# Kernel tuning notes

Hardware: AMD Instinct MI355X
Metric: run time of the kernel (lower is better)

Reference implementation:

```python
import jax, jax.numpy as jnp
import numpy as np

B, T, S, K, H, V = 8, 100, 400, 8, 512, 32000

def setup_inputs() -> dict:
    key = jax.random.key(0)
    ks = jax.random.split(key, 8)
    return {
        "dec_out": jax.random.normal(ks[0], (B, T, H), jnp.float32),
        "W": jax.random.normal(ks[1], (H, V), jnp.float32) * (1.0 / np.sqrt(H)),
        "b": jnp.zeros((V,), jnp.float32),
        "weights": jax.random.uniform(ks[2], (B, T, S), jnp.float32),
        "p_trans": jax.random.uniform(ks[3], (B, T, 1), jnp.float32),
        "trans_probs": jax.random.uniform(ks[4], (B, S, K), jnp.float32),
        "probs": jax.random.uniform(ks[5], (B, S, K), jnp.float32),
        "idxes": jax.random.randint(ks[6], (B, S, K), 0, V, jnp.int64),
    }

def reference(dec_out, W, b, weights, p_trans, trans_probs, probs, idxes):
    # Generator: linear + softmax over vocab -> (B, T, V)
    scores = jax.nn.softmax(jnp.einsum('bth,hv->btv', dec_out, W) + b, axis=-1)
    # Mask translation probs where source prob <= 0.05
    tp = trans_probs * (probs > 0.05).astype(trans_probs.dtype)  # (B, S, K)
    # scatter_add along vocab dim: tmp[b, s, idxes[b, s, k]] += tp[b, s, k]
    bi = jnp.arange(B)[:, None, None]
    si = jnp.arange(S)[None, :, None]
    tmp = jnp.zeros((B, S, V), dec_out.dtype).at[bi, si, idxes].add(tp)
    # blend copy distribution through attention weights
    trans_scores = jnp.einsum('bts,bsv->btv', weights, tmp)
    return jnp.log(p_trans * trans_scores + (1.0 - p_trans) * scores)
```

## Files before the change

kernel.cpp:

```cpp
#include <hip/hip_runtime.h>

#define Bdim 8
#define Tdim 100
#define Sdim 400
#define Kk   8
#define Hdim 512
#define Vdim 32000
#define Mdim 800
#define VHALF 16000

typedef __attribute__((ext_vector_type(8))) short short8;
typedef __attribute__((ext_vector_type(4))) float float4_t;

static __device__ __forceinline__ unsigned short f2bf(float f) {
    unsigned int x = __float_as_uint(f);
    return (unsigned short)((x + 0x7fffu + ((x >> 16) & 1u)) >> 16);
}
static __device__ __forceinline__ float bf2f(unsigned short h) {
    return __uint_as_float(((unsigned int)h) << 16);
}

static __device__ __forceinline__ void gload_lds16(const void* g, void* s) {
    __builtin_amdgcn_global_load_lds((const __attribute__((address_space(1))) void*)g,
                                     (__attribute__((address_space(3))) void*)s, 16, 0, 0);
}

__global__ void zero_kernel(float* __restrict__ p, int n) {
    int i = blockIdx.x * blockDim.x + threadIdx.x;
    if (i < n) p[i] = 0.f;
}

__global__ void convert_a_kernel(const float* __restrict__ A, unsigned short* __restrict__ Abf, int n) {
    int i = blockIdx.x * blockDim.x + threadIdx.x;
    if (i < n) Abf[i] = f2bf(A[i]);
}

__global__ void transpose_kernel(const float* __restrict__ W, unsigned short* __restrict__ WT) {
    __shared__ float tile[32][33];
    int k0 = blockIdx.y * 32;
    int v0 = blockIdx.x * 32;
    int tx = threadIdx.x & 31;
    int ty = threadIdx.x >> 5;
#pragma unroll
    for (int i = 0; i < 32; i += 8)
        tile[ty + i][tx] = W[(k0 + ty + i) * Vdim + v0 + tx];
    __syncthreads();
#pragma unroll
    for (int i = 0; i < 32; i += 8) {
        int v = v0 + ty + i;
        WT[v * Hdim + k0 + tx] = f2bf(tile[tx][ty + i]);
    }
}

__global__ __launch_bounds__(256) void gemm_kernel(const unsigned short* __restrict__ Abf,
                                                   const unsigned short* __restrict__ WT,
                                                   const float* __restrict__ bias,
                                                   unsigned short* __restrict__ logitsbf,
                                                   float* __restrict__ rowsum) {
    __shared__ __align__(16) unsigned short As[128 * 64];
    __shared__ __align__(16) unsigned short Bs[128 * 64];

    const int tid  = threadIdx.x;
    const int lane = tid & 63;
    const int wave = tid >> 6;
    const int l15  = lane & 15;
    const int kq   = lane >> 4;
    const int m_blk = blockIdx.x * 128;
    const int n_blk = blockIdx.y * 128;
    const int wm = wave & 1, wn = wave >> 1;
    const int m0 = wm * 64, n0 = wn * 64;

    const unsigned short* agp[4];
    const unsigned short* bgp[4];
    unsigned short* alp[4];
    unsigned short* blp[4];
#pragma unroll
    for (int q = 0; q < 4; ++q) {
        int chunk = (q * 4 + wave) * 64 + lane;
        int row = chunk >> 3, c = chunk & 7;
        int gc  = c ^ (row & 7);
        int arow = m_blk + row;
        if (arow >= Mdim) arow = Mdim - 1;
        agp[q] = Abf + (size_t)arow * Hdim + gc * 8;
        bgp[q] = WT + (size_t)(n_blk + row) * Hdim + gc * 8;
        alp[q] = As + (q * 4 + wave) * 512;
        blp[q] = Bs + (q * 4 + wave) * 512;
    }

    int a_off[2][4], b_off[2][4];
#pragma unroll
    for (int ks = 0; ks < 2; ++ks)
#pragma unroll
        for (int i = 0; i < 4; ++i) {
            int ra = m0 + i * 16 + l15;
            a_off[ks][i] = ra * 64 + (((ks * 4 + kq) ^ (ra & 7)) * 8);
            int rb = n0 + i * 16 + l15;
            b_off[ks][i] = rb * 64 + (((ks * 4 + kq) ^ (rb & 7)) * 8);
        }

    float4_t acc[4][4] = {};

    for (int kt = 0; kt < 8; ++kt) {
        if (kt) __syncthreads();
        const int ko = kt * 64;
#pragma unroll
        for (int q = 0; q < 4; ++q) {
            gload_lds16(agp[q] + ko, alp[q]);
            gload_lds16(bgp[q] + ko, blp[q]);
        }
        __syncthreads();
#pragma unroll
        for (int ks = 0; ks < 2; ++ks) {
            short8 af[4], bfr[4];
#pragma unroll
            for (int i = 0; i < 4; ++i) af[i]  = *(const short8*)(As + a_off[ks][i]);
#pragma unroll
            for (int j = 0; j < 4; ++j) bfr[j] = *(const short8*)(Bs + b_off[ks][j]);
#pragma unroll
            for (int i = 0; i < 4; ++i)
#pragma unroll
                for (int j = 0; j < 4; ++j)
                    acc[i][j] = __builtin_amdgcn_mfma_f32_16x16x32_bf16(af[i], bfr[j], acc[i][j], 0, 0, 0);
        }
    }

    float bj[4];
#pragma unroll
    for (int j = 0; j < 4; ++j) bj[j] = bias[n_blk + n0 + j * 16 + l15];

#pragma unroll
    for (int i = 0; i < 4; ++i) {
        float se[4] = {0.f, 0.f, 0.f, 0.f};
        int grow0 = m_blk + m0 + i * 16 + kq * 4;
#pragma unroll
        for (int j = 0; j < 4; ++j) {
            int col = n_blk + n0 + j * 16 + l15;
#pragma unroll
            for (int r = 0; r < 4; ++r) {
                float v = acc[i][j][r] + bj[j];
                se[r] += __expf(v);
                if (grow0 + r < Mdim)
                    logitsbf[(size_t)(grow0 + r) * Vdim + col] = f2bf(v);
            }
        }
#pragma unroll
        for (int r = 0; r < 4; ++r) {
#pragma unroll
            for (int off = 8; off; off >>= 1)
                se[r] += __shfl_xor(se[r], off, 64);
        }
        if (l15 == 0) {
#pragma unroll
            for (int r = 0; r < 4; ++r)
                if (grow0 + r < Mdim) atomicAdd(&rowsum[grow0 + r], se[r]);
        }
    }
}

__global__ __launch_bounds__(512) void combine_kernel(const unsigned short* __restrict__ logitsbf,
                                                      const float* __restrict__ weights,
                                                      const float* __restrict__ p_trans,
                                                      const float* __restrict__ trans_probs,
                                                      const float* __restrict__ probs,
                                                      const int* __restrict__ idxes,
                                                      const float* __restrict__ rowsum,
                                                      float* __restrict__ out) {
    __shared__ __align__(16) float ts[VHALF];

    int bt = blockIdx.x;
    int b  = bt / Tdim;
    int tid = threadIdx.x;

    float pt = p_trans[bt];
    float c1 = (1.f - pt) / rowsum[bt];

    const short8* lrow8 = (const short8*)(logitsbf + (size_t)bt * Vdim);
    float4* out4 = (float4*)(out + (size_t)bt * Vdim);
    float4* ts4  = (float4*)ts;

    for (int h = 0; h < 2; ++h) {
        float4 z = make_float4(0.f, 0.f, 0.f, 0.f);
        for (int i = tid; i < VHALF / 4; i += 512) ts4[i] = z;
        __syncthreads();

        for (int i = tid; i < Sdim * Kk; i += 512) {
            float pv  = probs[b * (Sdim * Kk) + i];
            float tpv = trans_probs[b * (Sdim * Kk) + i];
            int   idx = idxes[b * (Sdim * Kk) + i];
            int   rel = idx - h * VHALF;
            if (pv > 0.05f && (unsigned)rel < (unsigned)VHALF) {
                float w = weights[bt * Sdim + (i >> 3)];
                atomicAdd(&ts[rel], w * tpv);
            }
        }
        __syncthreads();

        for (int i = tid; i < VHALF / 8; i += 512) {
            short8 x8 = lrow8[h * (VHALF / 8) + i];
            float4 t0 = ts4[i * 2];
            float4 t1 = ts4[i * 2 + 1];
            float4 o0, o1;
            o0.x = __logf(pt * t0.x + c1 * __expf(bf2f((unsigned short)x8[0])));
            o0.y = __logf(pt * t0.y + c1 * __expf(bf2f((unsigned short)x8[1])));
            o0.z = __logf(pt * t0.z + c1 * __expf(bf2f((unsigned short)x8[2])));
            o0.w = __logf(pt * t0.w + c1 * __expf(bf2f((unsigned short)x8[3])));
            o1.x = __logf(pt * t1.x + c1 * __expf(bf2f((unsigned short)x8[4])));
            o1.y = __logf(pt * t1.y + c1 * __expf(bf2f((unsigned short)x8[5])));
            o1.z = __logf(pt * t1.z + c1 * __expf(bf2f((unsigned short)x8[6])));
            o1.w = __logf(pt * t1.w + c1 * __expf(bf2f((unsigned short)x8[7])));
            out4[(h * (VHALF / 8) + i) * 2]     = o0;
            out4[(h * (VHALF / 8) + i) * 2 + 1] = o1;
        }
        __syncthreads();
    }
}

extern "C" void kernel_launch(void* const* d_in, const int* in_sizes, int n_in,
                              void* d_out, int out_size, void* d_ws, size_t ws_size,
                              hipStream_t stream) {
    const float* dec_out     = (const float*)d_in[0];
    const float* W           = (const float*)d_in[1];
    const float* bias        = (const float*)d_in[2];
    const float* weights     = (const float*)d_in[3];
    const float* p_trans     = (const float*)d_in[4];
    const float* trans_probs = (const float*)d_in[5];
    const float* probs       = (const float*)d_in[6];
    const int*   idxes       = (const int*)d_in[7];
    float* out = (float*)d_out;

    char* wsb = (char*)d_ws;
    unsigned short* Abf      = (unsigned short*)wsb;
    unsigned short* WT       = (unsigned short*)(wsb + (1ull << 20));
    unsigned short* logitsbf = (unsigned short*)(wsb + (35ull << 20));
    float*          rowsum   = (float*)(wsb + (90ull << 20));

    zero_kernel<<<dim3(4), dim3(256), 0, stream>>>(rowsum, Mdim);
    convert_a_kernel<<<dim3((Mdim * Hdim + 255) / 256), dim3(256), 0, stream>>>(dec_out, Abf, Mdim * Hdim);
    transpose_kernel<<<dim3(Vdim / 32, Hdim / 32), dim3(256), 0, stream>>>(W, WT);
    gemm_kernel<<<dim3(7, Vdim / 128), dim3(256), 0, stream>>>(Abf, WT, bias, logitsbf, rowsum);
    combine_kernel<<<dim3(Mdim), dim3(512), 0, stream>>>(logitsbf, weights, p_trans, trans_probs,
                                                         probs, idxes, rowsum, out);
}
```

Baseline: 294.2 us.

## Keep full W tile resident in LDS and stream pre-packed A fragments

The GEMM now launches one block per 128-column vocab tile and loads the whole 128x512 bf16 W slice into LDS once (128 KB). It then loops over all 7 M tiles, reading A directly from global memory in a pre-packed MFMA fragment layout produced by a rewritten convert kernel. This removes the repeated W reloads across M blocks and the per-k-step barriers. The cost is only 250 blocks with very large LDS use, so occupancy is one block per CU. Separately, the combine kernel keeps the full 32000-float vocab row in LDS and does a single pass instead of two halves, which also needs a large LDS allocation.

New measurement: 478.0 us. +62.5%, slower.

```diff
diff --git a/kernel.cpp b/kernel.cpp
--- a/kernel.cpp
+++ b/kernel.cpp
@@ -7,7 +7,6 @@
 #define Hdim 512
 #define Vdim 32000
 #define Mdim 800
-#define VHALF 16000
 
 typedef __attribute__((ext_vector_type(8))) short short8;
 typedef __attribute__((ext_vector_type(4))) float float4_t;
@@ -30,9 +29,18 @@
     if (i < n) p[i] = 0.f;
 }
 
-__global__ void convert_a_kernel(const float* __restrict__ A, unsigned short* __restrict__ Abf, int n) {
-    int i = blockIdx.x * blockDim.x + threadIdx.x;
-    if (i < n) Abf[i] = f2bf(A[i]);
+__global__ void convert_a_kernel(const float* __restrict__ A, unsigned short* __restrict__ Ap) {
+    int tid = blockIdx.x * blockDim.x + threadIdx.x;
+    if (tid >= 50 * 1024) return;
+    int mt = tid >> 10;
+    int r  = tid & 1023;
+    int kc = r >> 4;
+    int l15 = r & 15;
+    const float* src = A + (size_t)(mt * 16 + l15) * Hdim + kc * 8;
+    short8 v;
+#pragma unroll
+    for (int j = 0; j < 8; ++j) v[j] = (short)f2bf(src[j]);
+    *(short8*)(Ap + (size_t)tid * 8) = v;
 }
 
 __global__ void transpose_kernel(const float* __restrict__ W, unsigned short* __restrict__ WT) {
@@ -43,116 +51,105 @@
     int ty = threadIdx.x >> 5;
 #pragma unroll
     for (int i = 0; i < 32; i += 8)
-        tile[ty + i][tx] = W[(k0 + ty + i) * Vdim + v0 + tx];
+        tile[ty + i][tx] = W[(size_t)(k0 + ty + i) * Vdim + v0 + tx];
     __syncthreads();
 #pragma unroll
     for (int i = 0; i < 32; i += 8) {
         int v = v0 + ty + i;
-        WT[v * Hdim + k0 + tx] = f2bf(tile[tx][ty + i]);
-    }
-}
-
-__global__ __launch_bounds__(256) void gemm_kernel(const unsigned short* __restrict__ Abf,
+        WT[(size_t)v * Hdim + k0 + tx] = f2bf(tile[tx][ty + i]);
+    }
+}
+
+__global__ __launch_bounds__(256) void gemm_kernel(const unsigned short* __restrict__ Ap,
                                                    const unsigned short* __restrict__ WT,
                                                    const float* __restrict__ bias,
                                                    unsigned short* __restrict__ logitsbf,
                                                    float* __restrict__ rowsum) {
-    __shared__ __align__(16) unsigned short As[128 * 64];
-    __shared__ __align__(16) unsigned short Bs[128 * 64];
+    __shared__ __align__(16) unsigned short Bs[128 * 512];
 
     const int tid  = threadIdx.x;
     const int lane = tid & 63;
     const int wave = tid >> 6;
     const int l15  = lane & 15;
     const int kq   = lane >> 4;
-    const int m_blk = blockIdx.x * 128;
-    const int n_blk = blockIdx.y * 128;
+    const int n_blk = blockIdx.x * 128;
     const int wm = wave & 1, wn = wave >> 1;
-    const int m0 = wm * 64, n0 = wn * 64;
-
-    const unsigned short* agp[4];
-    const unsigned short* bgp[4];
-    unsigned short* alp[4];
-    unsigned short* blp[4];
-#pragma unroll
-    for (int q = 0; q < 4; ++q) {
-        int chunk = (q * 4 + wave) * 64 + lane;
-        int row = chunk >> 3, c = chunk & 7;
-        int gc  = c ^ (row & 7);
-        int arow = m_blk + row;
-        if (arow >= Mdim) arow = Mdim - 1;
-        agp[q] = Abf + (size_t)arow * Hdim + gc * 8;
-        bgp[q] = WT + (size_t)(n_blk + row) * Hdim + gc * 8;
-        alp[q] = As + (q * 4 + wave) * 512;
-        blp[q] = Bs + (q * 4 + wave) * 512;
-    }
-
-    int a_off[2][4], b_off[2][4];
-#pragma unroll
-    for (int ks = 0; ks < 2; ++ks)
+    const int n0 = wn * 64;
+
+#pragma unroll 4
+    for (int it = 0; it < 32; ++it) {
+        int s = it * 256 + wave * 64 + lane;
+        int row = s >> 6, cs = s & 63;
+        int gc = (cs & 56) | ((cs & 7) ^ (row & 7));
+        gload_lds16(WT + (size_t)(n_blk + row) * Hdim + gc * 8,
+                    Bs + (size_t)(it * 256 + wave * 64) * 8);
+    }
+    __syncthreads();
+
+    int e0[4], e1[4];
+#pragma unroll
+    for (int j = 0; j < 4; ++j) {
+        int n = n0 + j * 16 + l15;
+        e0[j] = n * 512 + ((kq ^ (n & 7)) * 8);
+        e1[j] = n * 512 + (((4 + kq) ^ (n & 7)) * 8);
+    }
+
+    float bj[4];
+#pragma unroll
+    for (int j = 0; j < 4; ++j) bj[j] = bias[n_blk + n0 + j * 16 + l15];
+
+    for (int m_tile = 0; m_tile < 7; ++m_tile) {
+        const unsigned short* ap[4];
 #pragma unroll
         for (int i = 0; i < 4; ++i) {
-            int ra = m0 + i * 16 + l15;
-            a_off[ks][i] = ra * 64 + (((ks * 4 + kq) ^ (ra & 7)) * 8);
-            int rb = n0 + i * 16 + l15;
-            b_off[ks][i] = rb * 64 + (((ks * 4 + kq) ^ (rb & 7)) * 8);
-        }
-
-    float4_t acc[4][4] = {};
-
-    for (int kt = 0; kt < 8; ++kt) {
-        if (kt) __syncthreads();
-        const int ko = kt * 64;
-#pragma unroll
-        for (int q = 0; q < 4; ++q) {
-            gload_lds16(agp[q] + ko, alp[q]);
-            gload_lds16(bgp[q] + ko, blp[q]);
-        }
-        __syncthreads();
-#pragma unroll
-        for (int ks = 0; ks < 2; ++ks) {
+            int mt = m_tile * 8 + wm * 4 + i;
+            if (mt > 49) mt = 49;
+            ap[i] = Ap + (size_t)mt * 8192 + lane * 8;
+        }
+
+        float4_t acc[4][4] = {};
+#pragma unroll
+        for (int ks = 0; ks < 16; ++ks) {
             short8 af[4], bfr[4];
 #pragma unroll
-            for (int i = 0; i < 4; ++i) af[i]  = *(const short8*)(As + a_off[ks][i]);
-#pragma unroll
-            for (int j = 0; j < 4; ++j) bfr[j] = *(const short8*)(Bs + b_off[ks][j]);
+            for (int i = 0; i < 4; ++i) af[i] = *(const short8*)(ap[i] + ks * 512);
+            const int co = (ks >> 1) * 64;
+#pragma unroll
+            for (int j = 0; j < 4; ++j)
+                bfr[j] = *(const short8*)(Bs + ((ks & 1) ? e1[j] : e0[j]) + co);
 #pragma unroll
             for (int i = 0; i < 4; ++i)
 #pragma unroll
                 for (int j = 0; j < 4; ++j)
                     acc[i][j] = __builtin_amdgcn_mfma_f32_16x16x32_bf16(af[i], bfr[j], acc[i][j], 0, 0, 0);
         }
-    }
-
-    float bj[4];
-#pragma unroll
-    for (int j = 0; j < 4; ++j) bj[j] = bias[n_blk + n0 + j * 16 + l15];
-
-#pragma unroll
-    for (int i = 0; i < 4; ++i) {
-        float se[4] = {0.f, 0.f, 0.f, 0.f};
-        int grow0 = m_blk + m0 + i * 16 + kq * 4;
-#pragma unroll
-        for (int j = 0; j < 4; ++j) {
-            int col = n_blk + n0 + j * 16 + l15;
+
+#pragma unroll
+        for (int i = 0; i < 4; ++i) {
+            float se[4] = {0.f, 0.f, 0.f, 0.f};
+            int grow0 = m_tile * 128 + wm * 64 + i * 16 + kq * 4;
+#pragma unroll
+            for (int j = 0; j < 4; ++j) {
+                int col = n_blk + n0 + j * 16 + l15;
+#pragma unroll
+                for (int r = 0; r < 4; ++r) {
+                    float v = acc[i][j][r] + bj[j];
+                    se[r] += __expf(v);
+                    if (grow0 + r < Mdim)
+                        logitsbf[(size_t)(grow0 + r) * Vdim + col] = f2bf(v);
+                }
+            }
 #pragma unroll
             for (int r = 0; r < 4; ++r) {
-                float v = acc[i][j][r] + bj[j];
-                se[r] += __expf(v);
-                if (grow0 + r < Mdim)
-                    logitsbf[(size_t)(grow0 + r) * Vdim + col] = f2bf(v);
+#pragma unroll
+                for (int off = 8; off; off >>= 1)
+                    se[r] += __shfl_xor(se[r], off, 64);
             }
-        }
-#pragma unroll
-        for (int r = 0; r < 4; ++r) {
-#pragma unroll
-            for (int off = 8; off; off >>= 1)
-                se[r] += __shfl_xor(se[r], off, 64);
-        }
-        if (l15 == 0) {
-#pragma unroll
-            for (int r = 0; r < 4; ++r)
-                if (grow0 + r < Mdim) atomicAdd(&rowsum[grow0 + r], se[r]);
+            if (l15 == 0) {
+#pragma unroll
+                for (int r = 0; r < 4; ++r)
+                    if (grow0 + r < Mdim) atomicAdd(&rowsum[grow0 + r], se[r]);
+            }
         }
     }
 }
@@ -165,7 +162,7 @@
                                                       const int* __restrict__ idxes,
                                                       const float* __restrict__ rowsum,
                                                       float* __restrict__ out) {
-    __shared__ __align__(16) float ts[VHALF];
+    __shared__ __align__(16) float ts[Vdim];
 
     int bt = blockIdx.x;
     int b  = bt / Tdim;
@@ -178,40 +175,36 @@
     float4* out4 = (float4*)(out + (size_t)bt * Vdim);
     float4* ts4  = (float4*)ts;
 
-    for (int h = 0; h < 2; ++h) {
-        float4 z = make_float4(0.f, 0.f, 0.f, 0.f);
-        for (int i = tid; i < VHALF / 4; i += 512) ts4[i] = z;
-        __syncthreads();
-
-        for (int i = tid; i < Sdim * Kk; i += 512) {
-            float pv  = probs[b * (Sdim * Kk) + i];
-            float tpv = trans_probs[b * (Sdim * Kk) + i];
-            int   idx = idxes[b * (Sdim * Kk) + i];
-            int   rel = idx - h * VHALF;
-            if (pv > 0.05f && (unsigned)rel < (unsigned)VHALF) {
-                float w = weights[bt * Sdim + (i >> 3)];
-                atomicAdd(&ts[rel], w * tpv);
-            }
-        }
-        __syncthreads();
-
-        for (int i = tid; i < VHALF / 8; i += 512) {
-            short8 x8 = lrow8[h * (VHALF / 8) + i];
-            float4 t0 = ts4[i * 2];
-            float4 t1 = ts4[i * 2 + 1];
-            float4 o0, o1;
-            o0.x = __logf(pt * t0.x + c1 * __expf(bf2f((unsigned short)x8[0])));
-            o0.y = __logf(pt * t0.y + c1 * __expf(bf2f((unsigned short)x8[1])));
-            o0.z = __logf(pt * t0.z + c1 * __expf(bf2f((unsigned short)x8[2])));
-            o0.w = __logf(pt * t0.w + c1 * __expf(bf2f((unsigned short)x8[3])));
-            o1.x = __logf(pt * t1.x + c1 * __expf(bf2f((unsigned short)x8[4])));
-            o1.y = __logf(pt * t1.y + c1 * __expf(bf2f((unsigned short)x8[5])));
-            o1.z = __logf(pt * t1.z + c1 * __expf(bf2f((unsigned short)x8[6])));
-            o1.w = __logf(pt * t1.w + c1 * __expf(bf2f((unsigned short)x8[7])));
-            out4[(h * (VHALF / 8) + i) * 2]     = o0;
-            out4[(h * (VHALF / 8) + i) * 2 + 1] = o1;
-        }
-        __syncthreads();
+    float4 z = make_float4(0.f, 0.f, 0.f, 0.f);
+    for (int i = tid; i < Vdim / 4; i += 512) ts4[i] = z;
+    __syncthreads();
+
+    for (int i = tid; i < Sdim * Kk; i += 512) {
+        float pv  = probs[b * (Sdim * Kk) + i];
+        float tpv = trans_probs[b * (Sdim * Kk) + i];
+        int   idx = idxes[b * (Sdim * Kk) + i];
+        if (pv > 0.05f) {
+            float w = weights[bt * Sdim + (i >> 3)];
+            atomicAdd(&ts[idx], w * tpv);
+        }
+    }
+    __syncthreads();
+
+    for (int i = tid; i < Vdim / 8; i += 512) {
+        short8 x8 = lrow8[i];
+        float4 t0 = ts4[i * 2];
+        float4 t1 = ts4[i * 2 + 1];
+        float4 o0, o1;
+        o0.x = __logf(pt * t0.x + c1 * __expf(bf2f((unsigned short)x8[0])));
+        o0.y = __logf(pt * t0.y + c1 * __expf(bf2f((unsigned short)x8[1])));
+        o0.z = __logf(pt * t0.z + c1 * __expf(bf2f((unsigned short)x8[2])));
+        o0.w = __logf(pt * t0.w + c1 * __expf(bf2f((unsigned short)x8[3])));
+        o1.x = __logf(pt * t1.x + c1 * __expf(bf2f((unsigned short)x8[4])));
+        o1.y = __logf(pt * t1.y + c1 * __expf(bf2f((unsigned short)x8[5])));
+        o1.z = __logf(pt * t1.z + c1 * __expf(bf2f((unsigned short)x8[6])));
+        o1.w = __logf(pt * t1.w + c1 * __expf(bf2f((unsigned short)x8[7])));
+        out4[i * 2]     = o0;
+        out4[i * 2 + 1] = o1;
     }
 }
 
@@ -229,15 +222,15 @@
     float* out = (float*)d_out;
 
     char* wsb = (char*)d_ws;
-    unsigned short* Abf      = (unsigned short*)wsb;
+    unsigned short* Ap       = (unsigned short*)wsb;
     unsigned short* WT       = (unsigned short*)(wsb + (1ull << 20));
     unsigned short* logitsbf = (unsigned short*)(wsb + (35ull << 20));
     float*          rowsum   = (float*)(wsb + (90ull << 20));
 
     zero_kernel<<<dim3(4), dim3(256), 0, stream>>>(rowsum, Mdim);
-    convert_a_kernel<<<dim3((Mdim * Hdim + 255) / 256), dim3(256), 0, stream>>>(dec_out, Abf, Mdim * Hdim);
+    convert_a_kernel<<<dim3(200), dim3(256), 0, stream>>>(dec_out, Ap);
     transpose_kernel<<<dim3(Vdim / 32, Hdim / 32), dim3(256), 0, stream>>>(W, WT);
-    gemm_kernel<<<dim3(7, Vdim / 128), dim3(256), 0, stream>>>(Abf, WT, bias, logitsbf, rowsum);
+    gemm_kernel<<<dim3(Vdim / 128), dim3(256), 0, stream>>>(Ap, WT, bias, logitsbf, rowsum);
     combine_kernel<<<dim3(Mdim), dim3(512), 0, stream>>>(logitsbf, weights, p_trans, trans_probs,
                                                          probs, idxes, rowsum, out);
 }
```
